# Performance work log

Measured on AMD Instinct MI355X. Metric: run time of the kernel, lower is better.

## Reference

```python
import jax, jax.numpy as jnp
import numpy as np


def setup_inputs() -> dict:
    key = jax.random.key(0)
    ks = jax.random.split(key, 9)
    B, D, E, H, C = 8192, 1024, 8, 4096, 10
    s = lambda fan_in: 1.0 / np.sqrt(fan_in)
    return {
        "x":  jax.random.normal(ks[0], (B, D), jnp.float32),
        "Wr": jax.random.normal(ks[1], (D, E), jnp.float32) * s(D),
        "br": jnp.zeros((E,), jnp.float32),
        "W1": jax.random.normal(ks[2], (E, D, H), jnp.float32) * s(D),
        "b1": jnp.zeros((E, H), jnp.float32),
        "W2": jax.random.normal(ks[3], (E, H, D), jnp.float32) * s(H),
        "b2": jnp.zeros((E, D), jnp.float32),
        "Wc": jax.random.normal(ks[4], (D, C), jnp.float32) * s(D),
        "bc": jnp.zeros((C,), jnp.float32),
    }


def reference(x, Wr, br, W1, b1, W2, b2, Wc, bc):
    # Dense (no-topology) MoE path: softmax routing over all experts.
    routing = jax.nn.softmax(x @ Wr + br, axis=-1)          # [B, E]
    # All experts run on every token (dense all-expert loop, vectorized).
    h = jax.nn.relu(jnp.einsum('bd,edh->ebh', x, W1) + b1[:, None, :])  # [E, B, H]
    y = jnp.einsum('ebh,ehd->ebd', h, W2) + b2[:, None, :]              # [E, B, D]
    # Routing-weighted accumulation: sum_e y[e] * routing[:, e]
    out = jnp.einsum('ebd,be->bd', y, routing)              # [B, D]
    return out @ Wc + bc                                    # [B, C]
```

## Files before the change

### kernel.cpp

```cpp
#include <hip/hip_runtime.h>
#include <cstdint>
#include <cstddef>

using bf16x8 = __attribute__((ext_vector_type(8))) short;
using f32x4  = __attribute__((ext_vector_type(4))) float;

constexpr int kB = 8192;
constexpr int kD = 1024;
constexpr int kE = 8;
constexpr int kH = 4096;
constexpr int kC = 10;

__device__ __forceinline__ unsigned short f2bf(float f) {
  unsigned int u = __float_as_uint(f);
  u += 0x7FFFu + ((u >> 16) & 1u);
  return (unsigned short)(u >> 16);
}

#define GLD16(gptr, lptr)                                                      \
  __builtin_amdgcn_global_load_lds(                                            \
      (const __attribute__((address_space(1))) void*)(gptr),                   \
      (__attribute__((address_space(3))) void*)(lptr), 16, 0, 0)

__global__ __launch_bounds__(256) void k_prep(const float* __restrict__ x,
                                              const float* __restrict__ Wr,
                                              const float* __restrict__ br,
                                              const float* __restrict__ b2,
                                              const float* __restrict__ Wc,
                                              unsigned short* __restrict__ xb,
                                              float* __restrict__ r,
                                              float* __restrict__ part,
                                              float* __restrict__ u) {
  const int bid = blockIdx.x;
  const int t = threadIdx.x;
  if (bid < 4096) {
    const long i = ((long)bid * 256 + t) * 8;
    float4 a = *reinterpret_cast<const float4*>(x + i);
    float4 b = *reinterpret_cast<const float4*>(x + i + 4);
    bf16x8 o;
    o[0] = (short)f2bf(a.x); o[1] = (short)f2bf(a.y);
    o[2] = (short)f2bf(a.z); o[3] = (short)f2bf(a.w);
    o[4] = (short)f2bf(b.x); o[5] = (short)f2bf(b.y);
    o[6] = (short)f2bf(b.z); o[7] = (short)f2bf(b.w);
    *reinterpret_cast<bf16x8*>(xb + i) = o;
  } else if (bid < 6144) {
    const int w = t >> 6, l = t & 63;
    const int b = (bid - 4096) * 4 + w;
    const float* xr = x + (size_t)b * kD;
    float acc[kE];
#pragma unroll
    for (int e = 0; e < kE; ++e) acc[e] = 0.f;
    for (int d = l; d < kD; d += 64) {
      const float xv = xr[d];
      const float* wrow = Wr + d * kE;
#pragma unroll
      for (int e = 0; e < kE; ++e) acc[e] += xv * wrow[e];
    }
#pragma unroll
    for (int e = 0; e < kE; ++e) {
#pragma unroll
      for (int s = 32; s > 0; s >>= 1) acc[e] += __shfl_xor(acc[e], s);
      acc[e] += br[e];
    }
    float mx = acc[0];
#pragma unroll
    for (int e = 1; e < kE; ++e) mx = fmaxf(mx, acc[e]);
    float sum = 0.f;
#pragma unroll
    for (int e = 0; e < kE; ++e) { acc[e] = expf(acc[e] - mx); sum += acc[e]; }
    const float inv = 1.f / sum;
    float val = 0.f;
#pragma unroll
    for (int e = 0; e < kE; ++e) if (l == e) val = acc[e] * inv;
    if (l < kE) r[(size_t)b * kE + l] = val;
  } else if (bid < 6656) {
    part[(size_t)(bid - 6144) * 256 + t] = 0.f;
  } else {
    if (t >= kE * kC) return;
    const int e = t / kC, c = t % kC;
    float acc = 0.f;
    for (int d = 0; d < kD; ++d) acc += b2[e * kD + d] * Wc[d * kC + c];
    u[e * 16 + c] = acc;
  }
}

__global__ __launch_bounds__(256) void k_transpose_w(const float* __restrict__ W,
                                                     unsigned short* __restrict__ Wt,
                                                     int K, int N) {
  __shared__ unsigned short tile[32][33];
  const int e = blockIdx.z;
  const int n0 = blockIdx.x * 32, k0 = blockIdx.y * 32;
  const int tx = threadIdx.x, ty = threadIdx.y;
  const float* Wb = W + (size_t)e * K * N;
  unsigned short* Wtb = Wt + (size_t)e * N * K;
#pragma unroll
  for (int j = 0; j < 32; j += 8)
    tile[ty + j][tx] = f2bf(Wb[(size_t)(k0 + ty + j) * N + n0 + tx]);
  __syncthreads();
#pragma unroll
  for (int j = 0; j < 32; j += 8)
    Wtb[(size_t)(n0 + ty + j) * K + k0 + tx] = tile[tx][ty + j];
}

__global__ __launch_bounds__(128) void k_vbuild(const float* __restrict__ W2,
                                                const float* __restrict__ Wc,
                                                unsigned short* __restrict__ Vt) {
  __shared__ float WcL[kD * kC];
  for (int i = threadIdx.x; i < kD * kC; i += 128) WcL[i] = Wc[i];
  __syncthreads();
  const int gid = blockIdx.x * 128 + threadIdx.x;
  const int e = gid >> 12, hrow = gid & 4095;
  const float4* w2row = reinterpret_cast<const float4*>(W2 + (size_t)gid * kD);
  float acc[kC];
#pragma unroll
  for (int c = 0; c < kC; ++c) acc[c] = 0.f;
  for (int i = 0; i < kD / 4; ++i) {
    float4 w = w2row[i];
    const float* wc0 = WcL + (i * 4) * kC;
#pragma unroll
    for (int c = 0; c < kC; ++c)
      acc[c] += w.x * wc0[c] + w.y * wc0[kC + c] + w.z * wc0[2 * kC + c] +
                w.w * wc0[3 * kC + c];
  }
  unsigned short* vte = Vt + (size_t)e * 16 * kH;
#pragma unroll
  for (int c = 0; c < kC; ++c) vte[(size_t)c * kH + hrow] = f2bf(acc[c]);
#pragma unroll
  for (int c = kC; c < 16; ++c) vte[(size_t)c * kH + hrow] = 0;
}

__global__ __launch_bounds__(512, 2) void k_moe_fused256(
    const unsigned short* __restrict__ xb,
    const unsigned short* __restrict__ W1t,
    const float* __restrict__ b1,
    const unsigned short* __restrict__ Vt,
    const float* __restrict__ rr,
    float* __restrict__ part) {
  __shared__ __align__(16) char smem[131072];
  constexpr int K = kD;
  constexpr int NIT = K / 128;

  const int e = blockIdx.z;
  const int bx = (blockIdx.x & 7) * 4 + (blockIdx.x >> 3);
  const int brow = bx * 256, bcol = blockIdx.y * 256;
  const unsigned short* const At = xb;
  const unsigned short* const Bt = W1t + (size_t)e * kH * kD;

  const int tid = threadIdx.x;
  const int w = tid >> 6, l = tid & 63;
  const int wr = w >> 2, wc = w & 3;
  const int fr = l & 15, jg = l >> 4;

  int ck[2];
#pragma unroll
  for (int k = 0; k < 2; ++k) ck[k] = (((k * 4 + jg) ^ (fr & 7)) << 4);
  const int abase = wr * 16384;
  const int bbase = 32768 + (wc >> 1) * 16384;
  const int brow0 = (wc & 1) * 64;

  const int p0 = w * 64 + l;
  const int rp = p0 >> 3;
  const int cs = (p0 & 7) ^ (rp & 7);
  const size_t aofs = (size_t)(brow + rp) * K + cs * 8;
  const size_t bofs = (size_t)(bcol + rp) * K + cs * 8;
  const int ldst = w * 1024;

#define STG_A(buf, ht, kt)                                                     \
  do {                                                                         \
    GLD16(At + aofs + (size_t)(ht) * 131072 + (size_t)(kt) * 64,               \
          smem + (buf) * 65536 + (ht) * 16384 + ldst);                         \
    GLD16(At + aofs + (size_t)(ht) * 131072 + 65536 + (size_t)(kt) * 64,       \
          smem + (buf) * 65536 + (ht) * 16384 + 8192 + ldst);                  \
  } while (0)
#define STG_B(buf, ht, kt)                                                     \
  do {                                                                         \
    GLD16(Bt + bofs + (size_t)(ht) * 131072 + (size_t)(kt) * 64,               \
          smem + (buf) * 65536 + 32768 + (ht) * 16384 + ldst);                 \
    GLD16(Bt + bofs + (size_t)(ht) * 131072 + 65536 + (size_t)(kt) * 64,       \
          smem + (buf) * 65536 + 32768 + (ht) * 16384 + 8192 + ldst);          \
  } while (0)

#define READ_A(buf, mp)                                                        \
  do {                                                                         \
    _Pragma("unroll") for (int mm = 0; mm < 2; ++mm)                           \
    _Pragma("unroll") for (int k = 0; k < 2; ++k)                              \
      aq[mm][k] = *reinterpret_cast<const bf16x8*>(                            \
          smem + (buf) * 65536 + abase + (((mp) * 2 + mm) * 16 + fr) * 128 + ck[k]); \
  } while (0)
#define READ_B(buf)                                                            \
  do {                                                                         \
    _Pragma("unroll") for (int n = 0; n < 4; ++n)                              \
    _Pragma("unroll") for (int k = 0; k < 2; ++k)                              \
      bq[n][k] = *reinterpret_cast<const bf16x8*>(                             \
          smem + (buf) * 65536 + bbase + (brow0 + n * 16 + fr) * 128 + ck[k]); \
  } while (0)
#define MFMA16(mp)                                                             \
  do {                                                                         \
    __builtin_amdgcn_s_setprio(1);                                             \
    _Pragma("unroll") for (int mm = 0; mm < 2; ++mm)                           \
    _Pragma("unroll") for (int n = 0; n < 4; ++n)                              \
    _Pragma("unroll") for (int k = 0; k < 2; ++k)                              \
      acc[(mp) * 2 + mm][n] = __builtin_amdgcn_mfma_f32_16x16x32_bf16(         \
          aq[mm][k], bq[n][k], acc[(mp) * 2 + mm][n], 0, 0, 0);                \
    __builtin_amdgcn_s_setprio(0);                                             \
  } while (0)
#define BARP() asm volatile("s_barrier" ::: "memory")

  bf16x8 aq[2][2], bq[4][2];
  f32x4 acc[8][4];
#pragma unroll
  for (int m = 0; m < 8; ++m)
#pragma unroll
    for (int n = 0; n < 4; ++n) acc[m][n] = (f32x4){0.f, 0.f, 0.f, 0.f};

  STG_A(0, 0, 0); STG_A(0, 1, 0); STG_B(0, 0, 0); STG_B(0, 1, 0);
  STG_B(1, 0, 1); STG_B(1, 1, 1);
  asm volatile("s_waitcnt vmcnt(4)" ::: "memory");
  BARP();

  for (int i = 0; i < NIT; ++i) {
    const bool g = (i < NIT - 1);
    const int kx = 2 * i + 2, ky = 2 * i + 3;
    READ_A(0, 0); READ_B(0);
    STG_A(1, 0, 2 * i + 1);
    BARP(); MFMA16(0); BARP();
    READ_A(0, 1);
    STG_A(1, 1, 2 * i + 1);
    if (g) STG_B(0, 0, kx);
    BARP(); MFMA16(1); BARP();
    READ_A(0, 2);
    if (g) STG_B(0, 1, kx);
    BARP(); MFMA16(2); BARP();
    READ_A(0, 3);
    BARP(); MFMA16(3);
    if (g) asm volatile("s_waitcnt vmcnt(4)" ::: "memory");
    else   asm volatile("s_waitcnt vmcnt(0)" ::: "memory");
    BARP();
    READ_A(1, 0); READ_B(1);
    if (g) { STG_A(0, 0, kx); STG_A(0, 1, kx); }
    BARP(); MFMA16(0); BARP();
    READ_A(1, 1);
    if (g) STG_B(1, 0, ky);
    BARP(); MFMA16(1); BARP();
    READ_A(1, 2);
    if (g) STG_B(1, 1, ky);
    BARP(); MFMA16(2); BARP();
    READ_A(1, 3);
    BARP(); MFMA16(3);
    if (g) asm volatile("s_waitcnt vmcnt(4)" ::: "memory");
    BARP();
  }
#undef STG_A
#undef STG_B
#undef READ_A
#undef READ_B

#pragma unroll
  for (int n = 0; n < 4; ++n) {
    const int lcol = wc * 64 + n * 16 + fr;
    const float bias = b1[(size_t)e * kH + bcol + lcol];
    const int cbyte = (lcol >> 3) << 4;
#pragma unroll
    for (int m = 0; m < 8; ++m) {
#pragma unroll
      for (int j = 0; j < 4; ++j) {
        const int lrow = wr * 128 + m * 16 + jg * 4 + j;
        const float v = fmaxf(acc[m][n][j] + bias, 0.f);
        *reinterpret_cast<unsigned short*>(
            smem + lrow * 512 + (cbyte ^ ((lrow & 7) << 4)) + (fr & 7) * 2) = f2bf(v);
      }
    }
  }
  asm volatile("s_waitcnt lgkmcnt(0)\ns_barrier" ::: "memory");

  const unsigned short* const VtE = Vt + (size_t)e * 16 * kH + (size_t)fr * kH + bcol;
  bf16x8 gv[8];
#pragma unroll
  for (int kk = 0; kk < 8; ++kk)
    gv[kk] = *reinterpret_cast<const bf16x8*>(VtE + kk * 32 + jg * 8);
#pragma unroll
  for (int f = 0; f < 2; ++f) {
    const int rowl = (2 * w + f) * 16 + fr;
    f32x4 pc = (f32x4){0.f, 0.f, 0.f, 0.f};
#pragma unroll
    for (int kk = 0; kk < 8; ++kk) {
      bf16x8 ga = *reinterpret_cast<const bf16x8*>(
          smem + rowl * 512 + ((((kk * 4 + jg)) ^ (rowl & 7)) << 4));
      pc = __builtin_amdgcn_mfma_f32_16x16x32_bf16(ga, gv[kk], pc, 0, 0, 0);
    }
    const int rowg = brow + (2 * w + f) * 16 + jg * 4;
#pragma unroll
    for (int j = 0; j < 4; ++j) {
      const float val = pc[j] * rr[(size_t)(rowg + j) * kE + e];
      atomicAdd(&part[(size_t)(rowg + j) * 16 + fr], val);
    }
  }
#undef MFMA16
#undef BARP
}

__global__ __launch_bounds__(256) void k_combine(const float* __restrict__ part,
                                                 const float* __restrict__ rr,
                                                 const float* __restrict__ u,
                                                 const float* __restrict__ bc,
                                                 float* __restrict__ y) {
  const int tid = threadIdx.x;
  const int rloc = tid >> 4, c = tid & 15;
  const int b = blockIdx.x * 16 + rloc;
  if (c >= kC) return;
  float acc = part[(size_t)b * 16 + c] + bc[c];
#pragma unroll
  for (int e = 0; e < kE; ++e) acc += rr[(size_t)b * kE + e] * u[e * 16 + c];
  y[(size_t)b * kC + c] = acc;
}

extern "C" void kernel_launch(void* const* d_in, const int* in_sizes, int n_in,
                              void* d_out, int out_size, void* d_ws, size_t ws_size,
                              hipStream_t stream) {
  (void)in_sizes; (void)n_in; (void)out_size; (void)ws_size;
  const float* x  = (const float*)d_in[0];
  const float* Wr = (const float*)d_in[1];
  const float* br = (const float*)d_in[2];
  const float* W1 = (const float*)d_in[3];
  const float* b1 = (const float*)d_in[4];
  const float* W2 = (const float*)d_in[5];
  const float* b2 = (const float*)d_in[6];
  const float* Wc = (const float*)d_in[7];
  const float* bc = (const float*)d_in[8];
  float* y = (float*)d_out;

  char* p = (char*)d_ws;
  unsigned short* xb  = (unsigned short*)p; p += (size_t)kB * kD * 2;
  unsigned short* W1t = (unsigned short*)p; p += (size_t)kE * kH * kD * 2;
  unsigned short* Vt  = (unsigned short*)p; p += (size_t)kE * 16 * kH * 2;
  float* r    = (float*)p;                  p += (size_t)kB * kE * 4;
  float* u    = (float*)p;                  p += (size_t)kE * 16 * 4;
  float* part = (float*)p;                  p += (size_t)kB * 16 * 4;

  k_prep<<<dim3(6657), dim3(256), 0, stream>>>(x, Wr, br, b2, Wc, xb, r, part, u);
  k_transpose_w<<<dim3(kH / 32, kD / 32, kE), dim3(32, 8), 0, stream>>>(W1, W1t, kD, kH);
  k_vbuild<<<dim3(kE * kH / 128), dim3(128), 0, stream>>>(W2, Wc, Vt);

  k_moe_fused256<<<dim3(kB / 256, kH / 256, kE), dim3(512), 0, stream>>>(
      xb, W1t, b1, Vt, r, part);

  k_combine<<<dim3(kB / 16), dim3(256), 0, stream>>>(part, r, u, bc, y);
}
```

Before: 689.9 us.

## Load W1 fragments directly from global into registers, triple-buffer A tiles in LDS

The fused MoE GEMM no longer stages the weight (B) tile through shared memory. Each wave now loads its B fragments straight from global memory into registers one k-step ahead, while the activation (A) tile uses a three-stage LDS ring with prefetch distance two. This removes the LDS traffic and bandwidth for B and simplifies the barrier/waitcnt schedule. In exchange, B loads become per-lane strided global reads with no sharing between the two wave rows. The loop is also fully unrolled with a full vmcnt(0) wait every step, which may expose global latency and raise register pressure.

```diff
diff --git a/kernel.cpp b/kernel.cpp
--- a/kernel.cpp
+++ b/kernel.cpp
@@ -138,7 +138,7 @@
     float* __restrict__ part) {
   __shared__ __align__(16) char smem[131072];
   constexpr int K = kD;
-  constexpr int NIT = K / 128;
+  constexpr int NKT = K / 64;
 
   const int e = blockIdx.z;
   const int bx = (blockIdx.x & 7) * 4 + (blockIdx.x >> 3);
@@ -155,45 +155,39 @@
 #pragma unroll
   for (int k = 0; k < 2; ++k) ck[k] = (((k * 4 + jg) ^ (fr & 7)) << 4);
   const int abase = wr * 16384;
-  const int bbase = 32768 + (wc >> 1) * 16384;
-  const int brow0 = (wc & 1) * 64;
 
   const int p0 = w * 64 + l;
   const int rp = p0 >> 3;
   const int cs = (p0 & 7) ^ (rp & 7);
   const size_t aofs = (size_t)(brow + rp) * K + cs * 8;
-  const size_t bofs = (size_t)(bcol + rp) * K + cs * 8;
   const int ldst = w * 1024;
 
-#define STG_A(buf, ht, kt)                                                     \
+  const unsigned short* const Bw = Bt + (size_t)(bcol + wc * 64 + fr) * K + jg * 8;
+
+#define STGA(ao, kt)                                                           \
   do {                                                                         \
-    GLD16(At + aofs + (size_t)(ht) * 131072 + (size_t)(kt) * 64,               \
-          smem + (buf) * 65536 + (ht) * 16384 + ldst);                         \
-    GLD16(At + aofs + (size_t)(ht) * 131072 + 65536 + (size_t)(kt) * 64,       \
-          smem + (buf) * 65536 + (ht) * 16384 + 8192 + ldst);                  \
+    GLD16(At + aofs + (size_t)(kt) * 64,          smem + (ao) + ldst);         \
+    GLD16(At + aofs + 65536 + (size_t)(kt) * 64,  smem + (ao) + 8192 + ldst);  \
+    GLD16(At + aofs + 131072 + (size_t)(kt) * 64, smem + (ao) + 16384 + ldst); \
+    GLD16(At + aofs + 196608 + (size_t)(kt) * 64, smem + (ao) + 24576 + ldst); \
   } while (0)
-#define STG_B(buf, ht, kt)                                                     \
-  do {                                                                         \
-    GLD16(Bt + bofs + (size_t)(ht) * 131072 + (size_t)(kt) * 64,               \
-          smem + (buf) * 65536 + 32768 + (ht) * 16384 + ldst);                 \
-    GLD16(Bt + bofs + (size_t)(ht) * 131072 + 65536 + (size_t)(kt) * 64,       \
-          smem + (buf) * 65536 + 32768 + (ht) * 16384 + 8192 + ldst);          \
-  } while (0)
-
-#define READ_A(buf, mp)                                                        \
+
+#define READ_A(ao, mp)                                                         \
   do {                                                                         \
     _Pragma("unroll") for (int mm = 0; mm < 2; ++mm)                           \
     _Pragma("unroll") for (int k = 0; k < 2; ++k)                              \
       aq[mm][k] = *reinterpret_cast<const bf16x8*>(                            \
-          smem + (buf) * 65536 + abase + (((mp) * 2 + mm) * 16 + fr) * 128 + ck[k]); \
+          smem + (ao) + abase + (((mp) * 2 + mm) * 16 + fr) * 128 + ck[k]);    \
   } while (0)
-#define READ_B(buf)                                                            \
+
+#define LOADB(kt)                                                              \
   do {                                                                         \
     _Pragma("unroll") for (int n = 0; n < 4; ++n)                              \
     _Pragma("unroll") for (int k = 0; k < 2; ++k)                              \
       bq[n][k] = *reinterpret_cast<const bf16x8*>(                             \
-          smem + (buf) * 65536 + bbase + (brow0 + n * 16 + fr) * 128 + ck[k]); \
+          Bw + n * 16 * K + (kt) * 64 + k * 32);                               \
   } while (0)
+
 #define MFMA16(mp)                                                             \
   do {                                                                         \
     __builtin_amdgcn_s_setprio(1);                                             \
@@ -204,7 +198,8 @@
           aq[mm][k], bq[n][k], acc[(mp) * 2 + mm][n], 0, 0, 0);                \
     __builtin_amdgcn_s_setprio(0);                                             \
   } while (0)
-#define BARP() asm volatile("s_barrier" ::: "memory")
+#define BARP()  asm volatile("s_barrier" ::: "memory")
+#define VMC0()  asm volatile("s_waitcnt vmcnt(0)" ::: "memory")
 
   bf16x8 aq[2][2], bq[4][2];
   f32x4 acc[8][4];
@@ -213,47 +208,32 @@
 #pragma unroll
     for (int n = 0; n < 4; ++n) acc[m][n] = (f32x4){0.f, 0.f, 0.f, 0.f};
 
-  STG_A(0, 0, 0); STG_A(0, 1, 0); STG_B(0, 0, 0); STG_B(0, 1, 0);
-  STG_B(1, 0, 1); STG_B(1, 1, 1);
-  asm volatile("s_waitcnt vmcnt(4)" ::: "memory");
+  STGA(0, 0);
+  STGA(32768, 1);
+  LOADB(0);
+  VMC0();
   BARP();
 
-  for (int i = 0; i < NIT; ++i) {
-    const bool g = (i < NIT - 1);
-    const int kx = 2 * i + 2, ky = 2 * i + 3;
-    READ_A(0, 0); READ_B(0);
-    STG_A(1, 0, 2 * i + 1);
+#pragma unroll
+  for (int t = 0; t < NKT; ++t) {
+    const int ao = (t % 3) * 32768;
+    const int so = ((t + 2) % 3) * 32768;
+    READ_A(ao, 0);
+    VMC0();
+    if (t + 2 < NKT) STGA(so, t + 2);
     BARP(); MFMA16(0); BARP();
-    READ_A(0, 1);
-    STG_A(1, 1, 2 * i + 1);
-    if (g) STG_B(0, 0, kx);
+    READ_A(ao, 1);
     BARP(); MFMA16(1); BARP();
-    READ_A(0, 2);
-    if (g) STG_B(0, 1, kx);
+    READ_A(ao, 2);
     BARP(); MFMA16(2); BARP();
-    READ_A(0, 3);
+    READ_A(ao, 3);
     BARP(); MFMA16(3);
-    if (g) asm volatile("s_waitcnt vmcnt(4)" ::: "memory");
-    else   asm volatile("s_waitcnt vmcnt(0)" ::: "memory");
+    if (t + 1 < NKT) LOADB(t + 1);
     BARP();
-    READ_A(1, 0); READ_B(1);
-    if (g) { STG_A(0, 0, kx); STG_A(0, 1, kx); }
-    BARP(); MFMA16(0); BARP();
-    READ_A(1, 1);
-    if (g) STG_B(1, 0, ky);
-    BARP(); MFMA16(1); BARP();
-    READ_A(1, 2);
-    if (g) STG_B(1, 1, ky);
-    BARP(); MFMA16(2); BARP();
-    READ_A(1, 3);
-    BARP(); MFMA16(3);
-    if (g) asm volatile("s_waitcnt vmcnt(4)" ::: "memory");
-    BARP();
-  }
-#undef STG_A
-#undef STG_B
+  }
+#undef STGA
 #undef READ_A
-#undef READ_B
+#undef LOADB
 
 #pragma unroll
   for (int n = 0; n < 4; ++n) {
@@ -297,6 +277,7 @@
   }
 #undef MFMA16
 #undef BARP
+#undef VMC0
 }
 
 __global__ __launch_bounds__(256) void k_combine(const float* __restrict__ part,
```

New measurement: 1.084 ms. 1.57x slower.

## Loop over experts inside each block and prefetch next expert's tiles across the epilogue

Applied to the files above, without the earlier changes.

The grid drops its expert dimension, so each block now iterates over all eight experts for its (row, column) tile. It prefetches the first k-slices of the next expert's x and W1 tiles while the current expert's main loop finishes and its projection epilogue runs. The epilogue is split into two 128-column halves so it only needs 64KB of shared memory, leaving the other buffer free for the prefetch. This aims to hide pipeline fill and epilogue latency and cut launch tail effects, but the grid shrinks by a factor of eight (32×16 = 512 blocks), which reduces parallelism and may hurt occupancy balance across CUs.

```diff
diff --git a/kernel.cpp b/kernel.cpp
--- a/kernel.cpp
+++ b/kernel.cpp
@@ -140,11 +140,9 @@
   constexpr int K = kD;
   constexpr int NIT = K / 128;
 
-  const int e = blockIdx.z;
   const int bx = (blockIdx.x & 7) * 4 + (blockIdx.x >> 3);
   const int brow = bx * 256, bcol = blockIdx.y * 256;
   const unsigned short* const At = xb;
-  const unsigned short* const Bt = W1t + (size_t)e * kH * kD;
 
   const int tid = threadIdx.x;
   const int w = tid >> 6, l = tid & 63;
@@ -162,7 +160,7 @@
   const int rp = p0 >> 3;
   const int cs = (p0 & 7) ^ (rp & 7);
   const size_t aofs = (size_t)(brow + rp) * K + cs * 8;
-  const size_t bofs = (size_t)(bcol + rp) * K + cs * 8;
+  const size_t bofs0 = (size_t)(bcol + rp) * K + cs * 8;
   const int ldst = w * 1024;
 
 #define STG_A(buf, ht, kt)                                                     \
@@ -172,11 +170,11 @@
     GLD16(At + aofs + (size_t)(ht) * 131072 + 65536 + (size_t)(kt) * 64,       \
           smem + (buf) * 65536 + (ht) * 16384 + 8192 + ldst);                  \
   } while (0)
-#define STG_B(buf, ht, kt)                                                     \
-  do {                                                                         \
-    GLD16(Bt + bofs + (size_t)(ht) * 131072 + (size_t)(kt) * 64,               \
+#define STG_B(BP, buf, ht, kt)                                                 \
+  do {                                                                         \
+    GLD16((BP) + bofs0 + (size_t)(ht) * 131072 + (size_t)(kt) * 64,            \
           smem + (buf) * 65536 + 32768 + (ht) * 16384 + ldst);                 \
-    GLD16(Bt + bofs + (size_t)(ht) * 131072 + 65536 + (size_t)(kt) * 64,       \
+    GLD16((BP) + bofs0 + (size_t)(ht) * 131072 + 65536 + (size_t)(kt) * 64,    \
           smem + (buf) * 65536 + 32768 + (ht) * 16384 + 8192 + ldst);          \
   } while (0)
 
@@ -204,99 +202,128 @@
           aq[mm][k], bq[n][k], acc[(mp) * 2 + mm][n], 0, 0, 0);                \
     __builtin_amdgcn_s_setprio(0);                                             \
   } while (0)
-#define BARP() asm volatile("s_barrier" ::: "memory")
+#define BARP()  asm volatile("s_barrier" ::: "memory")
+#define VM0()   asm volatile("s_waitcnt vmcnt(0)" ::: "memory")
+#define VM4()   asm volatile("s_waitcnt vmcnt(4)" ::: "memory")
+#define VM12()  asm volatile("s_waitcnt vmcnt(12)" ::: "memory")
 
   bf16x8 aq[2][2], bq[4][2];
   f32x4 acc[8][4];
-#pragma unroll
-  for (int m = 0; m < 8; ++m)
-#pragma unroll
-    for (int n = 0; n < 4; ++n) acc[m][n] = (f32x4){0.f, 0.f, 0.f, 0.f};
-
-  STG_A(0, 0, 0); STG_A(0, 1, 0); STG_B(0, 0, 0); STG_B(0, 1, 0);
-  STG_B(1, 0, 1); STG_B(1, 1, 1);
-  asm volatile("s_waitcnt vmcnt(4)" ::: "memory");
-  BARP();
-
-  for (int i = 0; i < NIT; ++i) {
-    const bool g = (i < NIT - 1);
-    const int kx = 2 * i + 2, ky = 2 * i + 3;
-    READ_A(0, 0); READ_B(0);
-    STG_A(1, 0, 2 * i + 1);
-    BARP(); MFMA16(0); BARP();
-    READ_A(0, 1);
-    STG_A(1, 1, 2 * i + 1);
-    if (g) STG_B(0, 0, kx);
-    BARP(); MFMA16(1); BARP();
-    READ_A(0, 2);
-    if (g) STG_B(0, 1, kx);
-    BARP(); MFMA16(2); BARP();
-    READ_A(0, 3);
-    BARP(); MFMA16(3);
-    if (g) asm volatile("s_waitcnt vmcnt(4)" ::: "memory");
-    else   asm volatile("s_waitcnt vmcnt(0)" ::: "memory");
+
+  for (int e = 0; e < kE; ++e) {
+    const unsigned short* const Bt  = W1t + (size_t)e * kH * kD;
+    const unsigned short* const BtN = W1t + (size_t)(e + 1) * kH * kD;
+    const bool more = (e + 1 < kE);
+#pragma unroll
+    for (int m = 0; m < 8; ++m)
+#pragma unroll
+      for (int n = 0; n < 4; ++n) acc[m][n] = (f32x4){0.f, 0.f, 0.f, 0.f};
+
+    if (e == 0) {
+      STG_A(0, 0, 0); STG_A(0, 1, 0);
+      STG_B(Bt, 0, 0, 0); STG_B(Bt, 0, 1, 0);
+      STG_B(Bt, 1, 0, 1); STG_B(Bt, 1, 1, 1);
+      VM4();
+    } else {
+      STG_B(Bt, 1, 0, 1); STG_B(Bt, 1, 1, 1);
+      VM12();
+    }
     BARP();
-    READ_A(1, 0); READ_B(1);
-    if (g) { STG_A(0, 0, kx); STG_A(0, 1, kx); }
-    BARP(); MFMA16(0); BARP();
-    READ_A(1, 1);
-    if (g) STG_B(1, 0, ky);
-    BARP(); MFMA16(1); BARP();
-    READ_A(1, 2);
-    if (g) STG_B(1, 1, ky);
-    BARP(); MFMA16(2); BARP();
-    READ_A(1, 3);
-    BARP(); MFMA16(3);
-    if (g) asm volatile("s_waitcnt vmcnt(4)" ::: "memory");
-    BARP();
+
+    for (int i = 0; i < NIT; ++i) {
+      const bool g = (i < NIT - 1);
+      const int kx = 2 * i + 2, ky = 2 * i + 3;
+      READ_A(0, 0); READ_B(0);
+      STG_A(1, 0, 2 * i + 1); STG_A(1, 1, 2 * i + 1);
+      BARP(); MFMA16(0); BARP();
+      READ_A(0, 1);
+      if (g) STG_B(Bt, 0, 0, kx);
+      BARP(); MFMA16(1); BARP();
+      READ_A(0, 2);
+      if (g) STG_B(Bt, 0, 1, kx);
+      BARP(); MFMA16(2); BARP();
+      READ_A(0, 3);
+      BARP(); MFMA16(3);
+      if (g) VM4(); else VM0();
+      BARP();
+      READ_A(1, 0); READ_B(1);
+      if (g)          { STG_A(0, 0, kx); STG_A(0, 1, kx); }
+      else if (more)  { STG_A(0, 0, 0);  STG_A(0, 1, 0);  }
+      BARP(); MFMA16(0); BARP();
+      READ_A(1, 1);
+      if (g)          STG_B(Bt, 1, 0, ky);
+      else if (more)  STG_B(BtN, 0, 0, 0);
+      BARP(); MFMA16(1); BARP();
+      READ_A(1, 2);
+      if (g)          STG_B(Bt, 1, 1, ky);
+      else if (more)  STG_B(BtN, 0, 1, 0);
+      BARP(); MFMA16(2); BARP();
+      READ_A(1, 3);
+      BARP(); MFMA16(3);
+      if (g) VM4();
+      BARP();
+    }
+
+    const unsigned short* const VtE = Vt + (size_t)e * 16 * kH + (size_t)fr * kH + bcol;
+    f32x4 pc[2];
+    pc[0] = (f32x4){0.f, 0.f, 0.f, 0.f};
+    pc[1] = (f32x4){0.f, 0.f, 0.f, 0.f};
+#pragma unroll
+    for (int h = 0; h < 2; ++h) {
+      if ((wc >> 1) == h) {
+#pragma unroll
+        for (int n = 0; n < 4; ++n) {
+          const int lcolH = (wc & 1) * 64 + n * 16 + fr;
+          const float bias = b1[(size_t)e * kH + bcol + h * 128 + lcolH];
+          const int cb = (lcolH >> 3) << 4;
+#pragma unroll
+          for (int m = 0; m < 8; ++m) {
+#pragma unroll
+            for (int j = 0; j < 4; ++j) {
+              const int lrow = wr * 128 + m * 16 + jg * 4 + j;
+              const float v = fmaxf(acc[m][n][j] + bias, 0.f);
+              *reinterpret_cast<unsigned short*>(
+                  smem + 65536 + lrow * 256 + (cb ^ ((lrow & 7) << 4)) + (fr & 7) * 2) = f2bf(v);
+            }
+          }
+        }
+      }
+      asm volatile("s_waitcnt lgkmcnt(0)\ns_barrier" ::: "memory");
+      bf16x8 gv[4];
+#pragma unroll
+      for (int kk = 0; kk < 4; ++kk)
+        gv[kk] = *reinterpret_cast<const bf16x8*>(VtE + h * 128 + kk * 32 + jg * 8);
+#pragma unroll
+      for (int f = 0; f < 2; ++f) {
+        const int rowl = (2 * w + f) * 16 + fr;
+#pragma unroll
+        for (int kk = 0; kk < 4; ++kk) {
+          bf16x8 ga = *reinterpret_cast<const bf16x8*>(
+              smem + 65536 + rowl * 256 + (((kk * 4 + jg) ^ (rowl & 7)) << 4));
+          pc[f] = __builtin_amdgcn_mfma_f32_16x16x32_bf16(ga, gv[kk], pc[f], 0, 0, 0);
+        }
+      }
+      BARP();
+    }
+#pragma unroll
+    for (int f = 0; f < 2; ++f) {
+      const int rowg = brow + (2 * w + f) * 16 + jg * 4;
+#pragma unroll
+      for (int j = 0; j < 4; ++j) {
+        const float val = pc[f][j] * rr[(size_t)(rowg + j) * kE + e];
+        atomicAdd(&part[(size_t)(rowg + j) * 16 + fr], val);
+      }
+    }
   }
 #undef STG_A
 #undef STG_B
 #undef READ_A
 #undef READ_B
-
-#pragma unroll
-  for (int n = 0; n < 4; ++n) {
-    const int lcol = wc * 64 + n * 16 + fr;
-    const float bias = b1[(size_t)e * kH + bcol + lcol];
-    const int cbyte = (lcol >> 3) << 4;
-#pragma unroll
-    for (int m = 0; m < 8; ++m) {
-#pragma unroll
-      for (int j = 0; j < 4; ++j) {
-        const int lrow = wr * 128 + m * 16 + jg * 4 + j;
-        const float v = fmaxf(acc[m][n][j] + bias, 0.f);
-        *reinterpret_cast<unsigned short*>(
-            smem + lrow * 512 + (cbyte ^ ((lrow & 7) << 4)) + (fr & 7) * 2) = f2bf(v);
-      }
-    }
-  }
-  asm volatile("s_waitcnt lgkmcnt(0)\ns_barrier" ::: "memory");
-
-  const unsigned short* const VtE = Vt + (size_t)e * 16 * kH + (size_t)fr * kH + bcol;
-  bf16x8 gv[8];
-#pragma unroll
-  for (int kk = 0; kk < 8; ++kk)
-    gv[kk] = *reinterpret_cast<const bf16x8*>(VtE + kk * 32 + jg * 8);
-#pragma unroll
-  for (int f = 0; f < 2; ++f) {
-    const int rowl = (2 * w + f) * 16 + fr;
-    f32x4 pc = (f32x4){0.f, 0.f, 0.f, 0.f};
-#pragma unroll
-    for (int kk = 0; kk < 8; ++kk) {
-      bf16x8 ga = *reinterpret_cast<const bf16x8*>(
-          smem + rowl * 512 + ((((kk * 4 + jg)) ^ (rowl & 7)) << 4));
-      pc = __builtin_amdgcn_mfma_f32_16x16x32_bf16(ga, gv[kk], pc, 0, 0, 0);
-    }
-    const int rowg = brow + (2 * w + f) * 16 + jg * 4;
-#pragma unroll
-    for (int j = 0; j < 4; ++j) {
-      const float val = pc[j] * rr[(size_t)(rowg + j) * kE + e];
-      atomicAdd(&part[(size_t)(rowg + j) * 16 + fr], val);
-    }
-  }
 #undef MFMA16
 #undef BARP
+#undef VM0
+#undef VM4
+#undef VM12
 }
 
 __global__ __launch_bounds__(256) void k_combine(const float* __restrict__ part,
@@ -341,7 +368,7 @@
   k_transpose_w<<<dim3(kH / 32, kD / 32, kE), dim3(32, 8), 0, stream>>>(W1, W1t, kD, kH);
   k_vbuild<<<dim3(kE * kH / 128), dim3(128), 0, stream>>>(W2, Wc, Vt);
 
-  k_moe_fused256<<<dim3(kB / 256, kH / 256, kE), dim3(512), 0, stream>>>(
+  k_moe_fused256<<<dim3(kB / 256, kH / 256, 1), dim3(512), 0, stream>>>(
       xb, W1t, b1, Vt, r, part);
 
   k_combine<<<dim3(kB / 16), dim3(256), 0, stream>>>(part, r, u, bc, y);
```

Measured after the change: 1.498 ms. +117.2%, slower.
